# Optimization experiments

Hardware: AMD Instinct MI355X
Metric: run time of the kernel (lower is better)

The kernel has to match this reference:

```python
import jax, jax.numpy as jnp
import numpy as np

B, T, D, H, W = 2, 8192, 512, 8, 256
d = D // H  # 64
NC = T // W  # number of chunks (T divisible by W)


def setup_inputs() -> dict:
    key = jax.random.key(0)
    ks = jax.random.split(key, 9)
    s = 1.0 / np.sqrt(D).astype(np.float32)
    x = jax.random.normal(ks[0], (B, T, D), jnp.float32)
    Wq = jax.random.normal(ks[1], (D, D), jnp.float32) * s
    Wk = jax.random.normal(ks[2], (D, D), jnp.float32) * s
    Wv = jax.random.normal(ks[3], (D, D), jnp.float32) * s
    Wo = jax.random.normal(ks[4], (D, D), jnp.float32) * s
    bq = jax.random.normal(ks[5], (D,), jnp.float32) * 0.01
    bk = jax.random.normal(ks[6], (D,), jnp.float32) * 0.01
    bv = jax.random.normal(ks[7], (D,), jnp.float32) * 0.01
    bo = jax.random.normal(ks[8], (D,), jnp.float32) * 0.01
    return {"x": x, "Wq": Wq, "bq": bq, "Wk": Wk, "bk": bk,
            "Wv": Wv, "bv": bv, "Wo": Wo, "bo": bo}


def _local_attention(q, k, v):
    # q, k, v: [B, H, T, d]. Each W-sized query chunk attends to keys in
    # [chunk_start - W, chunk_end + W) -> a 3W window, masked at boundaries.
    qc = q.reshape(B, H, NC, W, d)
    pad = ((0, 0), (0, 0), (W, W), (0, 0))
    kp = jnp.pad(k, pad)
    vp = jnp.pad(v, pad)
    # window gather indices into padded sequence: [NC, 3W]
    pos = jnp.arange(NC)[:, None] * W + jnp.arange(3 * W)[None, :]
    kw = kp[:, :, pos, :]  # [B, H, NC, 3W, d]
    vw = vp[:, :, pos, :]  # [B, H, NC, 3W, d]
    valid = (pos >= W) & (pos < T + W)  # [NC, 3W] true for real (unpadded) keys
    scores = jnp.einsum('bhcqd,bhckd->bhcqk', qc, kw) * (d ** -0.5)
    scores = jnp.where(valid[None, None, :, None, :], scores, -jnp.inf)
    attn = jax.nn.softmax(scores, axis=-1)
    out = jnp.einsum('bhcqk,bhckd->bhcqd', attn, vw)
    return out.reshape(B, H, T, d)


def reference(x, Wq, bq, Wk, bk, Wv, bv, Wo, bo):
    # Linear = x @ W.T + b (torch nn.Linear convention)
    q = (x @ Wq.T + bq).reshape(B, T, H, d).transpose(0, 2, 1, 3)
    # k_proj / v_proj run under torch.no_grad() in the original
    k = jax.lax.stop_gradient(x @ Wk.T + bk).reshape(B, T, H, d).transpose(0, 2, 1, 3)
    v = jax.lax.stop_gradient(x @ Wv.T + bv).reshape(B, T, H, d).transpose(0, 2, 1, 3)
    out = _local_attention(q, k, v)           # [B, H, T, d]
    out = out.transpose(0, 2, 1, 3).reshape(B, T, D)
    return out @ Wo.T + bo
```

## Files before the change

kernel.cpp:

```cpp
#include <hip/hip_runtime.h>
#include <hip/hip_bf16.h>

typedef unsigned short u16;
typedef unsigned int   u32;
typedef __bf16 bf16x8 __attribute__((ext_vector_type(8)));
typedef float  f32x4  __attribute__((ext_vector_type(4)));

#define BB 2
#define TT 8192
#define DD 512
#define HH 8
#define WW 256
#define DH 64
#define NX 8388608
#define NW 262144

__device__ __forceinline__ float b2f(u16 u) {
    unsigned int x = ((unsigned int)u) << 16;
    return __builtin_bit_cast(float, x);
}
__device__ __forceinline__ u16 f2b(float f) {
    __bf16 h = (__bf16)f;
    return __builtin_bit_cast(u16, h);
}
__device__ __forceinline__ bf16x8 ldsfrag(const u16* p) {
    return *(const bf16x8*)p;
}
__device__ __forceinline__ f32x4 mfma16(bf16x8 a, bf16x8 b, f32x4 c) {
    return __builtin_amdgcn_mfma_f32_16x16x32_bf16(a, b, c, 0, 0, 0);
}

typedef __attribute__((address_space(1))) u32 gu32;
typedef __attribute__((address_space(3))) u32 lu32;
__device__ __forceinline__ void gl_lds(const u16* g, u16* l) {
    __builtin_amdgcn_global_load_lds((gu32*)g, (lu32*)l, 16, 0, 0);
}

__device__ __forceinline__ void cvt8(const void* s, u16* d, long i, int f) {
    if (f) {
        const u32* sp = (const u32*)s + i;
        uint4 a = *(const uint4*)(sp);
        uint4 b = *(const uint4*)(sp + 4);
        u16 o[8];
        o[0] = f2b(__builtin_bit_cast(float, a.x));
        o[1] = f2b(__builtin_bit_cast(float, a.y));
        o[2] = f2b(__builtin_bit_cast(float, a.z));
        o[3] = f2b(__builtin_bit_cast(float, a.w));
        o[4] = f2b(__builtin_bit_cast(float, b.x));
        o[5] = f2b(__builtin_bit_cast(float, b.y));
        o[6] = f2b(__builtin_bit_cast(float, b.z));
        o[7] = f2b(__builtin_bit_cast(float, b.w));
        *(uint4*)(d + i) = *(const uint4*)o;
    } else {
        *(uint4*)(d + i) = *(const uint4*)((const u16*)s + i);
    }
}

__global__ void convert_all(const void* x, const void* Wq, const void* bq,
                            const void* Wk, const void* bk, const void* Wv,
                            const void* bv, const void* Wo, const void* bo,
                            u16* __restrict__ xb, u16* __restrict__ Wcat,
                            u16* __restrict__ Wob, u16* __restrict__ bcat,
                            u16* __restrict__ bob, int* __restrict__ flagw)
{
    __shared__ int sflag;
    const int tid = threadIdx.x;
    if (tid == 0) sflag = 0;
    __syncthreads();
    int mybad = 0;
    for (int i = tid; i < 2048; i += 256) {
        float v = b2f(((const u16*)x)[i]);
        if (!(fabsf(v) < 100.f)) mybad = 1;
    }
    if (mybad) atomicOr(&sflag, 1);
    __syncthreads();
    const int f = sflag ? 1 : 0;
    if (blockIdx.x == 0 && tid == 0) *flagw = f;

    long i = ((long)blockIdx.x * 256 + tid) * 8;
    if (i < NX)            { cvt8(x,  xb,           i, f); return; }
    i -= NX;
    if (i < NW)            { cvt8(Wq, Wcat,         i, f); return; }
    i -= NW;
    if (i < NW)            { cvt8(Wk, Wcat + NW,    i, f); return; }
    i -= NW;
    if (i < NW)            { cvt8(Wv, Wcat + 2*NW,  i, f); return; }
    i -= NW;
    if (i < NW)            { cvt8(Wo, Wob,          i, f); return; }
    i -= NW;
    if (i < 512)           { cvt8(bq, bcat,         i, f); return; }
    i -= 512;
    if (i < 512)           { cvt8(bk, bcat + 512,   i, f); return; }
    i -= 512;
    if (i < 512)           { cvt8(bv, bcat + 1024,  i, f); return; }
    i -= 512;
    if (i < 512)           { cvt8(bo, bob,          i, f); }
}

__global__ __launch_bounds__(512, 2)
void gemm256(const u16* __restrict__ A, const u16* __restrict__ Bw,
             const u16* __restrict__ bias, void* __restrict__ out0,
             u16* __restrict__ out1, u16* __restrict__ out2,
             int mode, const int* __restrict__ flagp)
{
    __shared__ __align__(16) u16 AsF[3][256 * 64];
    __shared__ __align__(16) u16 BsF[3][128 * 64];

    const int tid  = threadIdx.x;
    const int lane = tid & 63;
    const int wv   = tid >> 6;
    const int col  = lane & 15;
    const int quad = lane >> 4;
    const int wm   = (wv >> 1) * 64;
    const int wn   = (wv & 1) * 64;
    const int m0   = blockIdx.x * 256;
    const int n0   = blockIdx.y * 128;

    f32x4 acc[4][4] = {};

    const int lr  = lane >> 3;
    const int lc  = lane & 7;
    const int cbs = lc ^ lr;

    auto STG = [&](int buf, int k0, int half) {
        #pragma unroll
        for (int i = 0; i < 2; i++) {
            const int g = wv * 4 + half * 2 + i;
            gl_lds(A + (size_t)(m0 + g * 8 + lr) * 512 + k0 + cbs * 8,
                   &AsF[buf][g * 512]);
        }
        const int g2 = wv * 2 + half;
        gl_lds(Bw + (size_t)(n0 + g2 * 8 + lr) * 512 + k0 + cbs * 8,
               &BsF[buf][g2 * 512]);
    };

    STG(0, 0, 0);  STG(0, 0, 1);
    STG(1, 64, 0); STG(1, 64, 1);
    asm volatile("s_waitcnt vmcnt(6)" ::: "memory");
    __builtin_amdgcn_s_barrier();
    __builtin_amdgcn_sched_barrier(0);

    #pragma unroll
    for (int t = 0; t < 8; t++) {
        const int p  = t % 3;
        const int q  = (t + 2) % 3;
        const int k2 = (t + 2) * 64;
        bf16x8 fa[2][4], fb[2][4];
        #pragma unroll
        for (int mi = 0; mi < 4; mi++)
            fa[0][mi] = ldsfrag(&AsF[p][(wm + mi * 16 + col) * 64 + ((0 + quad) ^ (col & 7)) * 8]);
        #pragma unroll
        for (int ni = 0; ni < 4; ni++)
            fb[0][ni] = ldsfrag(&BsF[p][(wn + ni * 16 + col) * 64 + ((0 + quad) ^ (col & 7)) * 8]);
        if (t < 6) STG(q, k2, 0);
        #pragma unroll
        for (int mi = 0; mi < 4; mi++)
            fa[1][mi] = ldsfrag(&AsF[p][(wm + mi * 16 + col) * 64 + ((4 + quad) ^ (col & 7)) * 8]);
        #pragma unroll
        for (int ni = 0; ni < 4; ni++)
            fb[1][ni] = ldsfrag(&BsF[p][(wn + ni * 16 + col) * 64 + ((4 + quad) ^ (col & 7)) * 8]);
        if (t < 6) STG(q, k2, 1);
        asm volatile("s_waitcnt lgkmcnt(0)" ::: "memory");
        __builtin_amdgcn_sched_barrier(0);
        __builtin_amdgcn_s_setprio(1);
        #pragma unroll
        for (int kk = 0; kk < 2; kk++)
            #pragma unroll
            for (int mi = 0; mi < 4; mi++)
                #pragma unroll
                for (int ni = 0; ni < 4; ni++)
                    acc[mi][ni] = mfma16(fa[kk][mi], fb[kk][ni], acc[mi][ni]);
        __builtin_amdgcn_s_setprio(0);
        if (t < 6)      asm volatile("s_waitcnt vmcnt(6)" ::: "memory");
        else if (t == 6) asm volatile("s_waitcnt vmcnt(0)" ::: "memory");
        if (t < 7) {
            __builtin_amdgcn_s_barrier();
            __builtin_amdgcn_sched_barrier(0);
        }
    }

    if (mode == 0) {
        #pragma unroll
        for (int ni = 0; ni < 4; ni++) {
            const int gn = n0 + wn + ni * 16 + col;
            const float bv = b2f(bias[gn]);
            const int seg = gn >> 9;
            #pragma unroll
            for (int mi = 0; mi < 4; mi++) {
                const int gmb = m0 + wm + mi * 16 + quad * 4;
                if (seg < 2) {
                    u16* dst = (seg == 0) ? (u16*)out0 : out1;
                    #pragma unroll
                    for (int r = 0; r < 4; r++)
                        dst[(size_t)(gmb + r) * 512 + (gn & 511)] = f2b(acc[mi][ni][r] + bv);
                } else {
                    const int d = gn & 63, hh = (gn >> 6) & 7;
                    const int bb = gmb >> 13, t = gmb & 8191;
                    u16 pb[4];
                    #pragma unroll
                    for (int r = 0; r < 4; r++) pb[r] = f2b(acc[mi][ni][r] + bv);
                    uint2 pk;
                    pk.x = pb[0] | ((u32)pb[1] << 16);
                    pk.y = pb[2] | ((u32)pb[3] << 16);
                    *(uint2*)&out2[((size_t)(bb * 8 + hh) * 64 + d) * 8192 + t] = pk;
                }
            }
        }
    } else {
        const int outf32 = *flagp;
        #pragma unroll
        for (int ni = 0; ni < 4; ni++) {
            const int gn = n0 + wn + ni * 16 + col;
            const float bv = b2f(bias[gn]);
            #pragma unroll
            for (int mi = 0; mi < 4; mi++) {
                #pragma unroll
                for (int r = 0; r < 4; r++) {
                    const int gm = m0 + wm + mi * 16 + quad * 4 + r;
                    const float v = acc[mi][ni][r] + bv;
                    if (outf32) ((float*)out0)[(size_t)gm * 512 + gn] = v;
                    else        ((u16*)out0)[(size_t)gm * 512 + gn]  = f2b(v);
                }
            }
        }
    }
}

__global__ __launch_bounds__(512, 4)
void attn_local(const u16* __restrict__ Qg, const u16* __restrict__ Kg,
                const u16* __restrict__ VTg, u16* __restrict__ Og)
{
    __shared__ __align__(16) u16 Ks[2][64 * 64];
    __shared__ __align__(16) u16 VTs[2][64 * 64];

    const int tid  = threadIdx.x;
    const int lane = tid & 63;
    const int wv   = tid >> 6;
    const int col  = lane & 15;
    const int quad = lane >> 4;

    const int idx = blockIdx.x;
    const int c = idx & 31;
    const int h = (idx >> 5) & 7;
    const int b = idx >> 8;

    const int t0 = c * WW;
    const int wq = wv * 32;

    const int sc_lo = (c == 0) ? 4 : 0;
    const int nsc   = (c == 0 || c == 31) ? 8 : 12;

    const int ldr = lane >> 3;
    const int ldc = lane & 7;

    bf16x8 qf[2][2];
    {
        const size_t qbase = ((size_t)(b * TT + t0 + wq + col)) * DD + h * DH + quad * 8;
        #pragma unroll
        for (int qi = 0; qi < 2; qi++)
            #pragma unroll
            for (int kk = 0; kk < 2; kk++)
                qf[qi][kk] = *(const bf16x8*)(Qg + qbase + (size_t)qi * 16 * DD + kk * 32);
    }

    f32x4 o[4][2] = {};
    float lsum[2] = {0.f, 0.f};

    {
        const int kstart = t0 - WW + sc_lo * 64;
        const int rr = wv * 8 + ldr;
        const int cb = ldc ^ (rr & 7);
        gl_lds(Kg  + ((size_t)(b * TT + kstart + rr)) * DD + h * DH + cb * 8,
               &Ks[0][wv * 512]);
        gl_lds(VTg + ((size_t)((b * HH + h) * DH + rr)) * TT + kstart + cb * 8,
               &VTs[0][wv * 512]);
    }

    for (int it = 0; it < nsc; it++) {
        __syncthreads();
        if (it + 1 < nsc) {
            const int kstart = t0 - WW + (sc_lo + it + 1) * 64;
            const int buf = (it + 1) & 1;
            const int rr = wv * 8 + ldr;
            const int cb = ldc ^ (rr & 7);
            gl_lds(Kg  + ((size_t)(b * TT + kstart + rr)) * DD + h * DH + cb * 8,
                   &Ks[buf][wv * 512]);
            gl_lds(VTg + ((size_t)((b * HH + h) * DH + rr)) * TT + kstart + cb * 8,
                   &VTs[buf][wv * 512]);
        }
        const u16* ks = &Ks[it & 1][0];
        const u16* vs = &VTs[it & 1][0];

        #pragma unroll
        for (int half = 0; half < 2; half++) {
            uint2 p2[2][2];
            #pragma unroll
            for (int nsl = 0; nsl < 2; nsl++) {
                const int ns = half * 2 + nsl;
                const int row = ns * 16 + col;
                bf16x8 ka0 = ldsfrag(&ks[row * 64 + ((0 + quad) ^ (col & 7)) * 8]);
                bf16x8 ka1 = ldsfrag(&ks[row * 64 + ((4 + quad) ^ (col & 7)) * 8]);
                #pragma unroll
                for (int qi = 0; qi < 2; qi++) {
                    f32x4 sv = (f32x4){0.f, 0.f, 0.f, 0.f};
                    sv = mfma16(ka0, qf[qi][0], sv);
                    sv = mfma16(ka1, qf[qi][1], sv);
                    u16 pb[4];
                    #pragma unroll
                    for (int r = 0; r < 4; r++) {
                        const float p = __expf(sv[r] * 0.125f);
                        pb[r] = f2b(p);
                        lsum[qi] += p;
                    }
                    p2[nsl][qi].x = pb[0] | ((u32)pb[1] << 16);
                    p2[nsl][qi].y = pb[2] | ((u32)pb[3] << 16);
                }
            }
            bf16x8 pf[2];
            #pragma unroll
            for (int qi = 0; qi < 2; qi++) {
                uint4 w;
                w.x = p2[0][qi].x; w.y = p2[0][qi].y;
                w.z = p2[1][qi].x; w.w = p2[1][qi].y;
                pf[qi] = __builtin_bit_cast(bf16x8, w);
            }
            const int glo = (half * 4 +     (quad >> 1)) ^ (col & 7);
            const int ghi = (half * 4 + 2 + (quad >> 1)) ^ (col & 7);
            const int hb  = (quad & 1) * 8;
            #pragma unroll
            for (int di = 0; di < 4; di++) {
                const char* rowp = (const char*)&vs[(di * 16 + col) * 64];
                uint2 lo = *(const uint2*)(rowp + glo * 16 + hb);
                uint2 hi = *(const uint2*)(rowp + ghi * 16 + hb);
                uint4 w4;
                w4.x = lo.x; w4.y = lo.y; w4.z = hi.x; w4.w = hi.y;
                bf16x8 va = __builtin_bit_cast(bf16x8, w4);
                #pragma unroll
                for (int qi = 0; qi < 2; qi++)
                    o[di][qi] = mfma16(va, pf[qi], o[di][qi]);
            }
        }
    }

    #pragma unroll
    for (int qi = 0; qi < 2; qi++) {
        float l = lsum[qi];
        l += __shfl_xor(l, 16);
        l += __shfl_xor(l, 32);
        lsum[qi] = 1.0f / l;
    }

    #pragma unroll
    for (int qi = 0; qi < 2; qi++) {
        const size_t ob = ((size_t)(b * TT + t0 + wq + qi * 16 + col)) * DD + h * DH + quad * 4;
        #pragma unroll
        for (int di = 0; di < 4; di++) {
            u16 pb[4];
            #pragma unroll
            for (int r = 0; r < 4; r++) pb[r] = f2b(o[di][qi][r] * lsum[qi]);
            uint2 pk;
            pk.x = pb[0] | ((u32)pb[1] << 16);
            pk.y = pb[2] | ((u32)pb[3] << 16);
            *(uint2*)&Og[ob + di * 16] = pk;
        }
    }
}

extern "C" void kernel_launch(void* const* d_in, const int* in_sizes, int n_in,
                              void* d_out, int out_size, void* d_ws, size_t ws_size,
                              hipStream_t stream)
{
    u16* ws   = (u16*)d_ws;
    u16* xb   = ws;
    u16* Wcat = xb + NX;
    u16* Wob  = Wcat + 3 * NW;
    u16* bcat = Wob + NW;
    u16* bob  = bcat + 1536;
    u16* qws  = bob + 512;
    u16* kws  = qws + NX;
    u16* vtws = kws + NX;
    u16* aws  = vtws + NX;
    int* flag = (int*)(aws + NX);

    convert_all<<<4609, 256, 0, stream>>>(
        d_in[0], d_in[1], d_in[2], d_in[3], d_in[4], d_in[5], d_in[6], d_in[7], d_in[8],
        xb, Wcat, Wob, bcat, bob, flag);

    gemm256<<<dim3(64, 12), 512, 0, stream>>>(xb, Wcat, bcat, qws, kws, vtws, 0, flag);
    attn_local<<<dim3(BB * HH * 32), 512, 0, stream>>>(qws, kws, vtws, aws);
    gemm256<<<dim3(64, 4), 512, 0, stream>>>(aws, Wob, bob, d_out, nullptr, nullptr, 1, flag);
}
```

Before: 192.9 us.

## Enlarge GEMM tile to 256x256 with double-buffered LDS staging

The projection GEMM tile grows from 256x128 to 256x256, so each wave now computes a 128x64 sub-tile with 8x4 accumulators. The LDS ring drops from three buffers to two, with a simpler wait-all-then-barrier schedule. The aim is more operand reuse per staged byte and fewer blocks reading the same A rows. In exchange, launch grids shrink: the QKV GEMM goes to 384 blocks and the output GEMM to only 128 blocks, fewer than the number of CUs. Register pressure rises and the load/compute overlap is shallower, so occupancy and latency hiding may suffer.

```diff
diff --git a/kernel.cpp b/kernel.cpp
--- a/kernel.cpp
+++ b/kernel.cpp
@@ -103,77 +103,68 @@
              u16* __restrict__ out1, u16* __restrict__ out2,
              int mode, const int* __restrict__ flagp)
 {
-    __shared__ __align__(16) u16 AsF[3][256 * 64];
-    __shared__ __align__(16) u16 BsF[3][128 * 64];
+    __shared__ __align__(16) u16 AsF[2][256 * 64];
+    __shared__ __align__(16) u16 BsF[2][256 * 64];
 
     const int tid  = threadIdx.x;
     const int lane = tid & 63;
     const int wv   = tid >> 6;
     const int col  = lane & 15;
     const int quad = lane >> 4;
-    const int wm   = (wv >> 1) * 64;
-    const int wn   = (wv & 1) * 64;
+    const int wm   = (wv & 1) * 128;
+    const int wn   = (wv >> 1) * 64;
     const int m0   = blockIdx.x * 256;
-    const int n0   = blockIdx.y * 128;
-
-    f32x4 acc[4][4] = {};
+    const int n0   = blockIdx.y * 256;
+
+    f32x4 acc[8][4] = {};
 
     const int lr  = lane >> 3;
     const int lc  = lane & 7;
     const int cbs = lc ^ lr;
 
-    auto STG = [&](int buf, int k0, int half) {
-        #pragma unroll
-        for (int i = 0; i < 2; i++) {
-            const int g = wv * 4 + half * 2 + i;
-            gl_lds(A + (size_t)(m0 + g * 8 + lr) * 512 + k0 + cbs * 8,
+    auto STG = [&](int buf, int k0) {
+        #pragma unroll
+        for (int i = 0; i < 4; i++) {
+            const int g = wv * 4 + i;
+            gl_lds(A  + (size_t)(m0 + g * 8 + lr) * 512 + k0 + cbs * 8,
                    &AsF[buf][g * 512]);
-        }
-        const int g2 = wv * 2 + half;
-        gl_lds(Bw + (size_t)(n0 + g2 * 8 + lr) * 512 + k0 + cbs * 8,
-               &BsF[buf][g2 * 512]);
+            gl_lds(Bw + (size_t)(n0 + g * 8 + lr) * 512 + k0 + cbs * 8,
+                   &BsF[buf][g * 512]);
+        }
     };
 
-    STG(0, 0, 0);  STG(0, 0, 1);
-    STG(1, 64, 0); STG(1, 64, 1);
-    asm volatile("s_waitcnt vmcnt(6)" ::: "memory");
+    STG(0, 0);
+    asm volatile("s_waitcnt vmcnt(0)" ::: "memory");
     __builtin_amdgcn_s_barrier();
     __builtin_amdgcn_sched_barrier(0);
 
     #pragma unroll
     for (int t = 0; t < 8; t++) {
-        const int p  = t % 3;
-        const int q  = (t + 2) % 3;
-        const int k2 = (t + 2) * 64;
-        bf16x8 fa[2][4], fb[2][4];
-        #pragma unroll
-        for (int mi = 0; mi < 4; mi++)
-            fa[0][mi] = ldsfrag(&AsF[p][(wm + mi * 16 + col) * 64 + ((0 + quad) ^ (col & 7)) * 8]);
-        #pragma unroll
-        for (int ni = 0; ni < 4; ni++)
-            fb[0][ni] = ldsfrag(&BsF[p][(wn + ni * 16 + col) * 64 + ((0 + quad) ^ (col & 7)) * 8]);
-        if (t < 6) STG(q, k2, 0);
-        #pragma unroll
-        for (int mi = 0; mi < 4; mi++)
-            fa[1][mi] = ldsfrag(&AsF[p][(wm + mi * 16 + col) * 64 + ((4 + quad) ^ (col & 7)) * 8]);
-        #pragma unroll
-        for (int ni = 0; ni < 4; ni++)
-            fb[1][ni] = ldsfrag(&BsF[p][(wn + ni * 16 + col) * 64 + ((4 + quad) ^ (col & 7)) * 8]);
-        if (t < 6) STG(q, k2, 1);
+        const int p = t & 1;
+        if (t < 7) STG(p ^ 1, (t + 1) * 64);
+        bf16x8 fa[2][8], fb[2][4];
+        #pragma unroll
+        for (int kk = 0; kk < 2; kk++) {
+            #pragma unroll
+            for (int mi = 0; mi < 8; mi++)
+                fa[kk][mi] = ldsfrag(&AsF[p][(wm + mi * 16 + col) * 64 + ((kk * 4 + quad) ^ (col & 7)) * 8]);
+            #pragma unroll
+            for (int ni = 0; ni < 4; ni++)
+                fb[kk][ni] = ldsfrag(&BsF[p][(wn + ni * 16 + col) * 64 + ((kk * 4 + quad) ^ (col & 7)) * 8]);
+        }
         asm volatile("s_waitcnt lgkmcnt(0)" ::: "memory");
         __builtin_amdgcn_sched_barrier(0);
         __builtin_amdgcn_s_setprio(1);
         #pragma unroll
         for (int kk = 0; kk < 2; kk++)
             #pragma unroll
-            for (int mi = 0; mi < 4; mi++)
+            for (int mi = 0; mi < 8; mi++)
                 #pragma unroll
                 for (int ni = 0; ni < 4; ni++)
                     acc[mi][ni] = mfma16(fa[kk][mi], fb[kk][ni], acc[mi][ni]);
         __builtin_amdgcn_s_setprio(0);
-        if (t < 6)      asm volatile("s_waitcnt vmcnt(6)" ::: "memory");
-        else if (t == 6) asm volatile("s_waitcnt vmcnt(0)" ::: "memory");
         if (t < 7) {
+            asm volatile("s_waitcnt vmcnt(0)" ::: "memory");
             __builtin_amdgcn_s_barrier();
             __builtin_amdgcn_sched_barrier(0);
         }
@@ -186,7 +177,7 @@
             const float bv = b2f(bias[gn]);
             const int seg = gn >> 9;
             #pragma unroll
-            for (int mi = 0; mi < 4; mi++) {
+            for (int mi = 0; mi < 8; mi++) {
                 const int gmb = m0 + wm + mi * 16 + quad * 4;
                 if (seg < 2) {
                     u16* dst = (seg == 0) ? (u16*)out0 : out1;
@@ -213,7 +204,7 @@
             const int gn = n0 + wn + ni * 16 + col;
             const float bv = b2f(bias[gn]);
             #pragma unroll
-            for (int mi = 0; mi < 4; mi++) {
+            for (int mi = 0; mi < 8; mi++) {
                 #pragma unroll
                 for (int r = 0; r < 4; r++) {
                     const int gm = m0 + wm + mi * 16 + quad * 4 + r;
@@ -386,7 +377,7 @@
         d_in[0], d_in[1], d_in[2], d_in[3], d_in[4], d_in[5], d_in[6], d_in[7], d_in[8],
         xb, Wcat, Wob, bcat, bob, flag);
 
-    gemm256<<<dim3(64, 12), 512, 0, stream>>>(xb, Wcat, bcat, qws, kws, vtws, 0, flag);
+    gemm256<<<dim3(64, 6), 512, 0, stream>>>(xb, Wcat, bcat, qws, kws, vtws, 0, flag);
     attn_local<<<dim3(BB * HH * 32), 512, 0, stream>>>(qws, kws, vtws, aws);
-    gemm256<<<dim3(64, 4), 512, 0, stream>>>(aws, Wob, bob, d_out, nullptr, nullptr, 1, flag);
-}
+    gemm256<<<dim3(64, 2), 512, 0, stream>>>(aws, Wob, bob, d_out, nullptr, nullptr, 1, flag);
+}
```

After: 228.1 us. +18.2%, slower.
